# Kernel tuning notes

Hardware: AMD Instinct MI355X
Metric: run time of the kernel (lower is better)

The kernel has to match this reference:

```python
import jax, jax.numpy as jnp
import numpy as np


def setup_inputs() -> dict:
    key = jax.random.key(0)
    ks = jax.random.split(key, 4)
    B, C, H, W = 16, 3, 256, 256
    n_steps, kO, k = 10, 2, 3
    CK = C * kO
    x = jax.random.normal(ks[0], (B, C, H, W), jnp.float32)
    kerK = jax.random.normal(ks[1], (n_steps, CK, 1, k, k), jnp.float32) * 0.3
    beta = jax.random.uniform(ks[2], (n_steps, 1, CK, 1, 1), jnp.float32, minval=0.01, maxval=0.1)
    rho = jax.random.uniform(ks[3], (n_steps, 1, CK, 1, 1), jnp.float32, minval=0.5, maxval=1.5)
    return {"x": x, "kerK": kerK, "beta": beta, "rho": rho}


def _dwconv(ker, x, pad):
    # depthwise 'same' cross-correlation (torch conv2d semantics)
    # ker: (CK,1,k,k), x: (B,CK,H,W) -> (B,CK,H,W)
    return jax.lax.conv_general_dilated(
        x, ker, (1, 1), [(pad, pad), (pad, pad)],
        dimension_numbers=("NCHW", "OIHW", "NCHW"),
        feature_group_count=x.shape[1])


def _psf2otf(ker, H, W):
    # ker: (C, kk, kk) with kk odd; shift center to origin, then FFT -> (C,H,W) complex
    C, kk, _ = ker.shape
    r = (kk - 1) // 2
    pad = jnp.zeros((C, H, W), ker.dtype).at[:, :kk, :kk].set(ker)
    pad = jnp.roll(pad, (-r, -r), axis=(-2, -1))
    return jnp.fft.fft2(pad)


def _tv_forward(x, kerK, beta, rho):
    B, C, H, W = x.shape
    n_steps, CK, _, k, _ = kerK.shape
    kO = CK // C
    kR = (k - 1) // 2
    f = x
    u = x                                        # state u init = input (loop(): u = x0)
    p = jnp.zeros((B, CK, H, W), x.dtype)        # auxiliary p ~= Du
    mu = jnp.zeros_like(p)                       # scaled multiplier
    for i in range(n_steps):                     # structural unroll over fixed n_steps
        K = kerK[i]                              # (CK,1,k,k)
        rh = rho[i]                              # (1,CK,1,1)
        gm = beta[i] / rho[i]                    # gamma = beta/rho (per step docstring)
        # kerW = rho * flip(K): adjoint D^T as correlation with flipped kernel
        kerW = rh.reshape(CK, 1, 1, 1) * K[:, :, ::-1, ::-1]
        # w1 = f + CKtoC(D^T (p - mu)); CKtoC sums groups of kO channels
        w1 = f + _dwconv(kerW, p - mu, kR).reshape(B, C, kO, H, W).sum(2)
        # K^T K: depthwise full autocorrelation of each kernel -> (CK, 2k-1, 2k-1)
        ktk = jax.lax.conv_general_dilated(
            K.transpose(1, 0, 2, 3), K, (1, 1), [(k - 1, k - 1)] * 2,
            dimension_numbers=("NCHW", "OIHW", "NCHW"),
            feature_group_count=CK)[0] * rh.reshape(CK, 1, 1)
        sktk = ktk.reshape(C, kO, 2 * k - 1, 2 * k - 1).sum(1)   # (C,kk,kk)
        kerH = sktk.at[:, k - 1, k - 1].add(1.0)                 # I + rho*K^T K
        otf = _psf2otf(kerH, H, W)                               # (C,H,W) complex
        # FFT Wiener-style solve: u = ifft( fft(w1) / OTF )
        u = jnp.fft.ifft2(jnp.fft.fft2(w1) / otf[None]).real
        # c = D u (depthwise corr on channel-repeated u)
        c = _dwconv(K, jnp.repeat(u, kO, axis=1), kR)
        v = c + mu
        p = jnp.sign(v) * jnp.maximum(jnp.abs(v) - gm, 0.0)      # soft-threshold
        mu = mu + c - p
    return u


def reference(x, kerK, beta, rho):
    return _tv_forward(x, kerK, beta, rho)
```

## Files before the change

### kernel.cpp

```cpp
#include <hip/hip_runtime.h>
#include <hip/hip_fp16.h>
#include <math.h>

#define BATCH 16
#define CH 3
#define CKCH 6
#define HH 256
#define WW 256
#define NSTEPS 10
#define SW 132
#define HSP (HH*SW)
#define NUNITS 1536
#define XN4 786432
#define IDX(i) ((i) ^ (((i) >> 4) & 15))

struct __align__(8) h4 { __half2 a, b; };

__device__ __forceinline__ float2 cmulf(float2 a, float2 b) {
  return make_float2(a.x * b.x - a.y * b.y, a.x * b.y + a.y * b.x);
}
__device__ __forceinline__ float4 h4tof4(h4 v) {
  float2 f0 = __half22float2(v.a), f1 = __half22float2(v.b);
  return make_float4(f0.x, f0.y, f1.x, f1.y);
}
__device__ __forceinline__ h4 f4toh4(float4 v) {
  h4 r;
  r.a = __float22half2_rn(make_float2(v.x, v.y));
  r.b = __float22half2_rn(make_float2(v.z, v.w));
  return r;
}

struct SmBig {
  __half su[12][264];
  __half sdm[2][10][264];
  float2 zz[4][256];
};

template <int INV>
__device__ __forceinline__ void wave_fft256(float2* buf, const float2* tw, int l) {
#pragma unroll
  for (int st = 0; st < 4; ++st) {
    int m = 1 << (2 * st);
    int r = l & (m - 1);
    int qm = l - r;
    float2 w1 = tw[qm], w2 = tw[qm + 64], w3 = tw[2 * qm];
    if (INV) { w1.y = -w1.y; w2.y = -w2.y; w3.y = -w3.y; }
    float2 x0 = buf[IDX(l)];
    float2 x1 = buf[IDX(l + 128)];
    float2 x2 = buf[IDX(l + 64)];
    float2 x3 = buf[IDX(l + 192)];
    __builtin_amdgcn_wave_barrier();
    float2 aA = make_float2(x0.x + x1.x, x0.y + x1.y);
    float2 bA = cmulf(w1, make_float2(x0.x - x1.x, x0.y - x1.y));
    float2 aB = make_float2(x2.x + x3.x, x2.y + x3.y);
    float2 bB = cmulf(w2, make_float2(x2.x - x3.x, x2.y - x3.y));
    int base = 4 * qm + r;
    buf[IDX(base)]         = make_float2(aA.x + aB.x, aA.y + aB.y);
    buf[IDX(base + 2 * m)] = cmulf(w3, make_float2(aA.x - aB.x, aA.y - aB.y));
    buf[IDX(base + m)]     = make_float2(bA.x + bB.x, bA.y + bB.y);
    buf[IDX(base + 3 * m)] = cmulf(w3, make_float2(bA.x - bB.x, bA.y - bB.y));
    __builtin_amdgcn_wave_barrier();
  }
}

__global__ __launch_bounds__(256, 4) void fb_init(const float4* __restrict__ x4,
                                                  __half* __restrict__ xh,
                                                  const float* __restrict__ kerK,
                                                  const float* __restrict__ rho,
                                                  float* __restrict__ HinvT) {
  __shared__ float ctab[256], kerH[25];
  int tid = threadIdx.x;
  for (int idx = blockIdx.x * 256 + tid; idx < XN4; idx += gridDim.x * 256)
    ((h4*)xh)[idx] = f4toh4(x4[idx]);
  ctab[tid] = cosf(6.283185307179586f * (float)tid / 256.0f);
  __syncthreads();
  for (int unit = blockIdx.x; unit < 30 * 129; unit += gridDim.x) {
    int kx = unit % 129, ic = unit / 129;
    int c = ic % CH, i = ic / CH;
    if (tid < 25) {
      int a = tid / 5, b2 = tid % 5;
      float s = (a == 2 && b2 == 2) ? 1.0f : 0.0f;
      for (int o = 0; o < 2; ++o) {
        int ck = c * 2 + o;
        const float* Kk = kerK + (i * CKCH + ck) * 9;
        float rh = rho[i * CKCH + ck];
        float ac = 0.f;
        for (int ty = 0; ty < 3; ++ty)
          for (int tx = 0; tx < 3; ++tx) {
            int ya2 = a - 2 + ty, xb = b2 - 2 + tx;
            if (ya2 >= 0 && ya2 < 3 && xb >= 0 && xb < 3)
              ac += Kk[ya2 * 3 + xb] * Kk[ty * 3 + tx];
          }
        s += rh * ac;
      }
      kerH[tid] = s;
    }
    __syncthreads();
    float acc = 0.f;
#pragma unroll
    for (int a = 0; a < 5; ++a)
#pragma unroll
      for (int b2 = 0; b2 < 5; ++b2)
        acc += kerH[a * 5 + b2] * ctab[(tid * (a - 2) + kx * (b2 - 2)) & 255];
    HinvT[((size_t)ic * 129 + kx) * 256 + tid] = 1.0f / (65536.0f * acc);
    __syncthreads();
  }
}

__global__ __launch_bounds__(256, 6) void fb_bigstep(
    int step, const __half* __restrict__ xh, const float* __restrict__ kerK,
    const float* __restrict__ beta, const float* __restrict__ rho,
    const __half2* __restrict__ specIn, const __half* __restrict__ muIn,
    __half* __restrict__ muOut, __half2* __restrict__ specOut) {
  __shared__ SmBig S;
  __shared__ float2 tw[128];
  int tid = threadIdx.x;
  if (tid < 128) {
    float sn, cs;
    sincosf(-6.283185307179586f * (float)tid / 256.0f, &sn, &cs);
    tw[tid] = make_float2(cs, sn);
  }
  int unit = blockIdx.x;
  int strip = unit & 31;
  int bc = unit >> 5;
  int c = bc % CH, b = bc / CH;
  int y0 = strip * 8;
  int u = tid >> 6, l = tid & 63;
  bool first = (step == 0);
  float2* Z = &S.zz[u][0];
  __syncthreads();

  if (!first) {
    for (int round = 0; round < 2; ++round) {
      int j = round * 4 + u;
      bool act = (j < 6);
      int ya = y0 - 2 + 2 * j;
      if (act && ya >= 0 && ya < HH) {
        const __half2* Ar = specIn + ((size_t)bc * HH + ya) * SW;
        const __half2* Br = Ar + SW;
#pragma unroll
        for (int h = 0; h < 2; ++h) {
          int t = l + h * 64;
          float2 A = __half22float2(Ar[t]), B = __half22float2(Br[t]);
          Z[IDX(t)] = make_float2(A.x - B.y, A.y + B.x);
          int mI = 128 - t;
          float2 Am = __half22float2(Ar[mI]), Bm = __half22float2(Br[mI]);
          float2 zh;
          if (t == 0) zh = make_float2(Am.x - Bm.y, Am.y + Bm.x);
          else        zh = make_float2(Am.x + Bm.y, Bm.x - Am.y);
          Z[IDX(t + 128)] = zh;
        }
        __builtin_amdgcn_wave_barrier();
        wave_fft256<1>(Z, tw, l);
        int r0 = 2 * j;
#pragma unroll
        for (int h = 0; h < 4; ++h) {
          int xx = l + h * 64;
          float2 z = Z[IDX(xx)];
          S.su[r0][4 + xx] = __float2half(z.x);
          S.su[r0 + 1][4 + xx] = __float2half(z.y);
        }
      } else if (act) {
        int r0 = 2 * j;
        for (int k2 = l; k2 < 264; k2 += 64) {
          S.su[r0][k2] = __float2half(0.f);
          S.su[r0 + 1][k2] = __float2half(0.f);
        }
      }
    }
    __syncthreads();

    bool muZero = (step == 1);
    int ps = step - 1;
#pragma unroll 1
    for (int it = 0; it < 5; ++it) {
      int task = it * 4 + u;
      int o = task / 10, rr = task % 10;
      int y = y0 - 1 + rr;
      int ck = c * 2 + o;
      float4 dq = make_float4(0.f, 0.f, 0.f, 0.f);
      if (y >= 0 && y < HH) {
        const float* Kp = kerK + (ps * CKCH + ck) * 9;
        float kk[9];
#pragma unroll
        for (int q = 0; q < 9; ++q) kk[q] = Kp[q];
        float gm = beta[ps * CKCH + ck] / rho[ps * CKCH + ck];
        float4 c4 = make_float4(0.f, 0.f, 0.f, 0.f);
#pragma unroll
        for (int dy = 0; dy < 3; ++dy) {
          float4 mid = h4tof4(*(const h4*)&S.su[rr + dy][4 + 4 * l]);
          float lft = __shfl_up(mid.w, 1); if (l == 0) lft = 0.f;
          float rgt = __shfl_down(mid.x, 1); if (l == 63) rgt = 0.f;
          float w0 = kk[dy * 3], w1 = kk[dy * 3 + 1], w2 = kk[dy * 3 + 2];
          c4.x += w0 * lft   + w1 * mid.x + w2 * mid.y;
          c4.y += w0 * mid.x + w1 * mid.y + w2 * mid.z;
          c4.z += w0 * mid.y + w1 * mid.z + w2 * mid.w;
          c4.w += w0 * mid.z + w1 * mid.w + w2 * rgt;
        }
        size_t gidx = (((size_t)b * CKCH + ck) * HH + y) * WW + 4 * l;
        float4 m4 = make_float4(0.f, 0.f, 0.f, 0.f);
        if (!muZero) m4 = h4tof4(*(const h4*)(muIn + gidx));
        float4 mn4;
        {
          float v = c4.x + m4.x, av = fabsf(v) - gm;
          float pn = (av > 0.f) ? ((v > 0.f) ? av : -av) : 0.f;
          mn4.x = m4.x + c4.x - pn; dq.x = pn - mn4.x;
        }
        {
          float v = c4.y + m4.y, av = fabsf(v) - gm;
          float pn = (av > 0.f) ? ((v > 0.f) ? av : -av) : 0.f;
          mn4.y = m4.y + c4.y - pn; dq.y = pn - mn4.y;
        }
        {
          float v = c4.z + m4.z, av = fabsf(v) - gm;
          float pn = (av > 0.f) ? ((v > 0.f) ? av : -av) : 0.f;
          mn4.z = m4.z + c4.z - pn; dq.z = pn - mn4.z;
        }
        {
          float v = c4.w + m4.w, av = fabsf(v) - gm;
          float pn = (av > 0.f) ? ((v > 0.f) ? av : -av) : 0.f;
          mn4.w = m4.w + c4.w - pn; dq.w = pn - mn4.w;
        }
        if (rr >= 1 && rr <= 8) *(h4*)(muOut + gidx) = f4toh4(mn4);
      }
      *(h4*)&S.sdm[o][rr][4 + 4 * l] = f4toh4(dq);
    }
  }
  __syncthreads();

  int ya = y0 + 2 * u;
  const h4* xa = (const h4*)(xh + ((size_t)(b * CH + c) * HH + ya) * WW);
  float4 va = h4tof4(xa[l]), vb = h4tof4(xa[64 + l]);
  if (!first) {
#pragma unroll
    for (int o = 0; o < 2; ++o) {
      int ck = c * 2 + o;
      float rh = rho[step * CKCH + ck];
      const float* Kk = kerK + (step * CKCH + ck) * 9;
      float kw[9];
#pragma unroll
      for (int dy = 0; dy < 3; ++dy)
#pragma unroll
        for (int dx = 0; dx < 3; ++dx)
          kw[dy * 3 + dx] = rh * Kk[(2 - dy) * 3 + (2 - dx)];
      float4 mid[4]; float lf[4], rg[4];
#pragma unroll
      for (int r4 = 0; r4 < 4; ++r4) {
        mid[r4] = h4tof4(*(const h4*)&S.sdm[o][2 * u + r4][4 + 4 * l]);
        lf[r4] = __shfl_up(mid[r4].w, 1); if (l == 0) lf[r4] = 0.f;
        rg[r4] = __shfl_down(mid[r4].x, 1); if (l == 63) rg[r4] = 0.f;
      }
#pragma unroll
      for (int dy = 0; dy < 3; ++dy) {
        float w0 = kw[dy * 3], w1 = kw[dy * 3 + 1], w2 = kw[dy * 3 + 2];
        va.x += w0 * lf[dy]     + w1 * mid[dy].x   + w2 * mid[dy].y;
        va.y += w0 * mid[dy].x  + w1 * mid[dy].y   + w2 * mid[dy].z;
        va.z += w0 * mid[dy].y  + w1 * mid[dy].z   + w2 * mid[dy].w;
        va.w += w0 * mid[dy].z  + w1 * mid[dy].w   + w2 * rg[dy];
        vb.x += w0 * lf[dy+1]    + w1 * mid[dy+1].x + w2 * mid[dy+1].y;
        vb.y += w0 * mid[dy+1].x + w1 * mid[dy+1].y + w2 * mid[dy+1].z;
        vb.z += w0 * mid[dy+1].y + w1 * mid[dy+1].z + w2 * mid[dy+1].w;
        vb.w += w0 * mid[dy+1].z + w1 * mid[dy+1].w + w2 * rg[dy+1];
      }
    }
  }
  Z[IDX(4 * l + 0)] = make_float2(va.x, vb.x);
  Z[IDX(4 * l + 1)] = make_float2(va.y, vb.y);
  Z[IDX(4 * l + 2)] = make_float2(va.z, vb.z);
  Z[IDX(4 * l + 3)] = make_float2(va.w, vb.w);
  __builtin_amdgcn_wave_barrier();
  wave_fft256<0>(Z, tw, l);
  __half2* Sa = specOut + ((size_t)bc * HH + ya) * SW;
  __half2* Sb = Sa + SW;
#pragma unroll
  for (int h = 0; h < 2; ++h) {
    int k = l + h * 64;
    int mI = (256 - k) & 255;
    float2 zk = Z[IDX(k)], zm = Z[IDX(mI)];
    Sa[k] = __float22half2_rn(make_float2(0.5f * (zk.x + zm.x), 0.5f * (zk.y - zm.y)));
    Sb[k] = __float22half2_rn(make_float2(0.5f * (zk.y + zm.y), 0.5f * (zm.x - zk.x)));
  }
  if (l == 0) {
    float2 z1 = Z[IDX(128)];
    Sa[128] = __float22half2_rn(make_float2(z1.x, 0.f));
    Sb[128] = __float22half2_rn(make_float2(z1.y, 0.f));
  }
}

__global__ __launch_bounds__(512) void fb_colfft(int step, __half2* __restrict__ spec,
                                                 const float* __restrict__ HinvT) {
  int g = blockIdx.x & 15;
  int bc = blockIdx.x >> 4;
  int c = bc % CH;
  int x0 = g * 8;
  __half2* f = spec + (size_t)bc * HSP;

  __shared__ float2 az[9][257];
  __shared__ float2 tw[128];
  int tid = threadIdx.x;
  if (tid < 128) {
    float sn, cs;
    sincosf(-6.283185307179586f * (float)tid / 256.0f, &sn, &cs);
    tw[tid] = make_float2(cs, sn);
  }
  int col8 = tid & 7;
  int rowq = tid >> 3;
#pragma unroll
  for (int rb = 0; rb < 4; ++rb) {
    int row = rb * 64 + rowq;
    az[col8][IDX(row)] = __half22float2(f[row * SW + x0 + col8]);
  }
  if (g == 0 && tid < 256) az[8][IDX(tid)] = __half22float2(f[tid * SW + 128]);
  __syncthreads();

  int u = tid >> 6, l = tid & 63;
  {
    int kx = x0 + u;
    float2* A = &az[u][0];
    wave_fft256<0>(A, tw, l);
    const float* T = HinvT + ((size_t)(step * CH + c) * 129 + kx) * 256;
#pragma unroll
    for (int h = 0; h < 4; ++h) {
      int idx = l + 64 * h;
      float tv = T[idx];
      float2 z = A[IDX(idx)];
      A[IDX(idx)] = make_float2(z.x * tv, z.y * tv);
    }
    __builtin_amdgcn_wave_barrier();
    wave_fft256<1>(A, tw, l);
  }
  if (g == 0 && u == 0) {
    float2* A = &az[8][0];
    wave_fft256<0>(A, tw, l);
    const float* T = HinvT + ((size_t)(step * CH + c) * 129 + 128) * 256;
#pragma unroll
    for (int h = 0; h < 4; ++h) {
      int idx = l + 64 * h;
      float tv = T[idx];
      float2 z = A[IDX(idx)];
      A[IDX(idx)] = make_float2(z.x * tv, z.y * tv);
    }
    __builtin_amdgcn_wave_barrier();
    wave_fft256<1>(A, tw, l);
  }
  __syncthreads();

#pragma unroll
  for (int rb = 0; rb < 4; ++rb) {
    int row = rb * 64 + rowq;
    f[row * SW + x0 + col8] = __float22half2_rn(az[col8][IDX(row)]);
  }
  if (g == 0 && tid < 256) f[tid * SW + 128] = __float22half2_rn(az[8][IDX(tid)]);
}

__global__ __launch_bounds__(256, 6) void fb_final(const __half2* __restrict__ spec,
                                                   float* __restrict__ out) {
  __shared__ SmBig S;
  __shared__ float2 tw[128];
  int tid = threadIdx.x;
  if (tid < 128) {
    float sn, cs;
    sincosf(-6.283185307179586f * (float)tid / 256.0f, &sn, &cs);
    tw[tid] = make_float2(cs, sn);
  }
  __syncthreads();
  int unit = blockIdx.x;
  int strip = unit & 31;
  int bc = unit >> 5;
  int y0 = strip * 8;
  int u = tid >> 6, l = tid & 63;
  float2* Z = &S.zz[u][0];
  int ya = y0 + 2 * u;
  const __half2* Ar = spec + ((size_t)bc * HH + ya) * SW;
  const __half2* Br = Ar + SW;
#pragma unroll
  for (int h = 0; h < 2; ++h) {
    int t = l + h * 64;
    float2 A = __half22float2(Ar[t]), B = __half22float2(Br[t]);
    Z[IDX(t)] = make_float2(A.x - B.y, A.y + B.x);
    int mI = 128 - t;
    float2 Am = __half22float2(Ar[mI]), Bm = __half22float2(Br[mI]);
    float2 zh;
    if (t == 0) zh = make_float2(Am.x - Bm.y, Am.y + Bm.x);
    else        zh = make_float2(Am.x + Bm.y, Bm.x - Am.y);
    Z[IDX(t + 128)] = zh;
  }
  __builtin_amdgcn_wave_barrier();
  wave_fft256<1>(Z, tw, l);
  float* oa = out + ((size_t)bc * HH + ya) * WW;
#pragma unroll
  for (int h = 0; h < 4; ++h) {
    int xx = l + h * 64;
    float2 z = Z[IDX(xx)];
    oa[xx] = z.x;
    oa[WW + xx] = z.y;
  }
}

extern "C" void kernel_launch(void* const* d_in, const int* in_sizes, int n_in,
                              void* d_out, int out_size, void* d_ws, size_t ws_size,
                              hipStream_t stream) {
  const float4* x4 = (const float4*)d_in[0];
  const float* kerK = (const float*)d_in[1];
  const float* beta = (const float*)d_in[2];
  const float* rho = (const float*)d_in[3];
  float* out = (float*)d_out;

  const size_t PMU = (size_t)BATCH * CKCH * HH * WW;
  const size_t SPL = (size_t)BATCH * CH * HSP;

  __half* muA = (__half*)d_ws;
  __half* muB = muA + PMU;
  __half2* specA = (__half2*)(muB + PMU);
  __half2* specB = specA + SPL;
  float* HinvT = (float*)(specB + SPL);
  __half* xh = (__half*)(HinvT + (size_t)30 * 129 * 256);

  fb_init<<<NUNITS, 256, 0, stream>>>(x4, xh, kerK, rho, HinvT);
  for (int i = 0; i < NSTEPS; ++i) {
    __half2* sIn = (i & 1) ? specA : specB;
    __half2* sOut = (i & 1) ? specB : specA;
    const __half* mi = (i & 1) ? muB : muA;
    __half* mo = (i & 1) ? muA : muB;
    fb_bigstep<<<NUNITS, 256, 0, stream>>>(i, xh, kerK, beta, rho, sIn, mi, mo, sOut);
    fb_colfft<<<48 * 16, 512, 0, stream>>>(i, sOut, HinvT);
  }
  fb_final<<<NUNITS, 256, 0, stream>>>(specB, out);
}
```

Before: 396.0 us.

## Fold init kernel into first bigstep and prefetch mu loads

```diff
diff --git a/kernel.cpp b/kernel.cpp
--- a/kernel.cpp
+++ b/kernel.cpp
@@ -11,7 +11,6 @@
 #define SW 132
 #define HSP (HH*SW)
 #define NUNITS 1536
-#define XN4 786432
 #define IDX(i) ((i) ^ (((i) >> 4) & 15))
 
 struct __align__(8) h4 { __half2 a, b; };
@@ -63,55 +62,12 @@
   }
 }
 
-__global__ __launch_bounds__(256, 4) void fb_init(const float4* __restrict__ x4,
-                                                  __half* __restrict__ xh,
-                                                  const float* __restrict__ kerK,
-                                                  const float* __restrict__ rho,
-                                                  float* __restrict__ HinvT) {
-  __shared__ float ctab[256], kerH[25];
-  int tid = threadIdx.x;
-  for (int idx = blockIdx.x * 256 + tid; idx < XN4; idx += gridDim.x * 256)
-    ((h4*)xh)[idx] = f4toh4(x4[idx]);
-  ctab[tid] = cosf(6.283185307179586f * (float)tid / 256.0f);
-  __syncthreads();
-  for (int unit = blockIdx.x; unit < 30 * 129; unit += gridDim.x) {
-    int kx = unit % 129, ic = unit / 129;
-    int c = ic % CH, i = ic / CH;
-    if (tid < 25) {
-      int a = tid / 5, b2 = tid % 5;
-      float s = (a == 2 && b2 == 2) ? 1.0f : 0.0f;
-      for (int o = 0; o < 2; ++o) {
-        int ck = c * 2 + o;
-        const float* Kk = kerK + (i * CKCH + ck) * 9;
-        float rh = rho[i * CKCH + ck];
-        float ac = 0.f;
-        for (int ty = 0; ty < 3; ++ty)
-          for (int tx = 0; tx < 3; ++tx) {
-            int ya2 = a - 2 + ty, xb = b2 - 2 + tx;
-            if (ya2 >= 0 && ya2 < 3 && xb >= 0 && xb < 3)
-              ac += Kk[ya2 * 3 + xb] * Kk[ty * 3 + tx];
-          }
-        s += rh * ac;
-      }
-      kerH[tid] = s;
-    }
-    __syncthreads();
-    float acc = 0.f;
-#pragma unroll
-    for (int a = 0; a < 5; ++a)
-#pragma unroll
-      for (int b2 = 0; b2 < 5; ++b2)
-        acc += kerH[a * 5 + b2] * ctab[(tid * (a - 2) + kx * (b2 - 2)) & 255];
-    HinvT[((size_t)ic * 129 + kx) * 256 + tid] = 1.0f / (65536.0f * acc);
-    __syncthreads();
-  }
-}
-
 __global__ __launch_bounds__(256, 6) void fb_bigstep(
-    int step, const __half* __restrict__ xh, const float* __restrict__ kerK,
-    const float* __restrict__ beta, const float* __restrict__ rho,
-    const __half2* __restrict__ specIn, const __half* __restrict__ muIn,
-    __half* __restrict__ muOut, __half2* __restrict__ specOut) {
+    int step, const float4* __restrict__ x4, __half* __restrict__ xh,
+    const float* __restrict__ kerK, const float* __restrict__ beta,
+    const float* __restrict__ rho, const __half2* __restrict__ specIn,
+    const __half* __restrict__ muIn, __half* __restrict__ muOut,
+    __half2* __restrict__ specOut, float* __restrict__ HinvT) {
   __shared__ SmBig S;
   __shared__ float2 tw[128];
   int tid = threadIdx.x;
@@ -129,6 +85,50 @@
   bool first = (step == 0);
   float2* Z = &S.zz[u][0];
   __syncthreads();
+
+  if (first) {
+    {
+      const float4* xsrc = x4 + ((size_t)bc * HH + y0) * 64;
+      h4* xdst = (h4*)xh + ((size_t)bc * HH + y0) * 64;
+      xdst[tid] = f4toh4(xsrc[tid]);
+      xdst[tid + 256] = f4toh4(xsrc[tid + 256]);
+    }
+    float* ctab = (float*)&S.su[0][0];
+    float* kerH = ctab + 256;
+    ctab[tid] = cosf(6.283185307179586f * (float)tid / 256.0f);
+    __syncthreads();
+    for (int u2 = blockIdx.x; u2 < 30 * 129; u2 += gridDim.x) {
+      int kx = u2 % 129, ic = u2 / 129;
+      int cc2 = ic % CH, i2 = ic / CH;
+      if (tid < 25) {
+        int a = tid / 5, b2 = tid % 5;
+        float s = (a == 2 && b2 == 2) ? 1.0f : 0.0f;
+        for (int o = 0; o < 2; ++o) {
+          int ck = cc2 * 2 + o;
+          const float* Kk = kerK + (i2 * CKCH + ck) * 9;
+          float rh = rho[i2 * CKCH + ck];
+          float ac = 0.f;
+          for (int ty = 0; ty < 3; ++ty)
+            for (int tx = 0; tx < 3; ++tx) {
+              int ya2 = a - 2 + ty, xb = b2 - 2 + tx;
+              if (ya2 >= 0 && ya2 < 3 && xb >= 0 && xb < 3)
+                ac += Kk[ya2 * 3 + xb] * Kk[ty * 3 + tx];
+            }
+          s += rh * ac;
+        }
+        kerH[tid] = s;
+      }
+      __syncthreads();
+      float acc = 0.f;
+#pragma unroll
+      for (int a = 0; a < 5; ++a)
+#pragma unroll
+        for (int b2 = 0; b2 < 5; ++b2)
+          acc += kerH[a * 5 + b2] * ctab[(tid * (a - 2) + kx * (b2 - 2)) & 255];
+      HinvT[((size_t)ic * 129 + kx) * 256 + tid] = 1.0f / (65536.0f * acc);
+      __syncthreads();
+    }
+  }
 
   if (!first) {
     for (int round = 0; round < 2; ++round) {
@@ -172,6 +172,20 @@
 
     bool muZero = (step == 1);
     int ps = step - 1;
+    h4 mpre[5];
+    if (!muZero) {
+#pragma unroll
+      for (int it = 0; it < 5; ++it) {
+        int task = it * 4 + u;
+        int o = task / 10, rr = task % 10;
+        int y = y0 - 1 + rr;
+        int ck = c * 2 + o;
+        if (y >= 0 && y < HH) {
+          size_t gidx = (((size_t)b * CKCH + ck) * HH + y) * WW + 4 * l;
+          mpre[it] = *(const h4*)(muIn + gidx);
+        }
+      }
+    }
 #pragma unroll 1
     for (int it = 0; it < 5; ++it) {
       int task = it * 4 + u;
@@ -198,8 +212,7 @@
           c4.w += w0 * mid.z + w1 * mid.w + w2 * rgt;
         }
         size_t gidx = (((size_t)b * CKCH + ck) * HH + y) * WW + 4 * l;
-        float4 m4 = make_float4(0.f, 0.f, 0.f, 0.f);
-        if (!muZero) m4 = h4tof4(*(const h4*)(muIn + gidx));
+        float4 m4 = muZero ? make_float4(0.f, 0.f, 0.f, 0.f) : h4tof4(mpre[it]);
         float4 mn4;
         {
           float v = c4.x + m4.x, av = fabsf(v) - gm;
@@ -229,9 +242,13 @@
   __syncthreads();
 
   int ya = y0 + 2 * u;
-  const h4* xa = (const h4*)(xh + ((size_t)(b * CH + c) * HH + ya) * WW);
-  float4 va = h4tof4(xa[l]), vb = h4tof4(xa[64 + l]);
-  if (!first) {
+  float4 va, vb;
+  if (first) {
+    const float4* xf = x4 + ((size_t)bc * HH + ya) * 64;
+    va = xf[l]; vb = xf[64 + l];
+  } else {
+    const h4* xa = (const h4*)(xh + ((size_t)bc * HH + ya) * WW);
+    va = h4tof4(xa[l]); vb = h4tof4(xa[64 + l]);
 #pragma unroll
     for (int o = 0; o < 2; ++o) {
       int ck = c * 2 + o;
@@ -416,13 +433,13 @@
   float* HinvT = (float*)(specB + SPL);
   __half* xh = (__half*)(HinvT + (size_t)30 * 129 * 256);
 
-  fb_init<<<NUNITS, 256, 0, stream>>>(x4, xh, kerK, rho, HinvT);
   for (int i = 0; i < NSTEPS; ++i) {
     __half2* sIn = (i & 1) ? specA : specB;
     __half2* sOut = (i & 1) ? specB : specA;
     const __half* mi = (i & 1) ? muB : muA;
     __half* mo = (i & 1) ? muA : muB;
-    fb_bigstep<<<NUNITS, 256, 0, stream>>>(i, xh, kerK, beta, rho, sIn, mi, mo, sOut);
+    fb_bigstep<<<NUNITS, 256, 0, stream>>>(i, x4, xh, kerK, beta, rho, sIn, mi, mo,
+                                           sOut, HinvT);
     fb_colfft<<<48 * 16, 512, 0, stream>>>(i, sOut, HinvT);
   }
   fb_final<<<NUNITS, 256, 0, stream>>>(specB, out);
```

Result: slower. 415.8 us (+5.0%).
